# Performance work log

Measured on AMD Instinct MI355X. Metric: run time of the kernel, lower is better.

The kernel has to match this reference:

```python
import jax, jax.numpy as jnp
import numpy as np

N, E, IN_C, HID_C, OUT_C = 50000, 800000, 64, 64, 8
NEG_SLOPE = 0.2


def setup_inputs() -> dict:
    key = jax.random.key(0)
    ks = jax.random.split(key, 12)
    return {
        "x": jax.random.normal(ks[0], (N, IN_C), dtype=jnp.float32),
        "edge_index": jax.random.randint(ks[1], (2, E), 0, N, dtype=jnp.int64),
        "edge_value": jax.random.uniform(ks[2], (E,), dtype=jnp.float32),
        "W1": jax.random.normal(ks[3], (IN_C, HID_C), dtype=jnp.float32) * 0.1,
        "a1_src": jax.random.normal(ks[4], (HID_C,), dtype=jnp.float32) * 0.1,
        "a1_dst": jax.random.normal(ks[5], (HID_C,), dtype=jnp.float32) * 0.1,
        "b1": jnp.zeros((HID_C,), dtype=jnp.float32),
        "W2": jax.random.normal(ks[6], (HID_C, OUT_C), dtype=jnp.float32) * 0.1,
        "a2_src": jax.random.normal(ks[7], (OUT_C,), dtype=jnp.float32) * 0.1,
        "a2_dst": jax.random.normal(ks[8], (OUT_C,), dtype=jnp.float32) * 0.1,
        "b2": jnp.zeros((OUT_C,), dtype=jnp.float32),
    }


def _rgat_conv(x, src, dst, edge_value, W, a_src, a_dst, b, n_nodes):
    # Linear transform: [N, out_c]
    h = x @ W
    # Per-node attention halves, gathered per edge -> per-edge logit
    e_src = h @ a_src  # [N]
    e_dst = h @ a_dst  # [N]
    logits = jax.nn.leaky_relu(e_src[src] + e_dst[dst], negative_slope=NEG_SLOPE)  # [E]
    # Segment softmax over destination neighborhoods (numerically stable)
    m = jax.ops.segment_max(logits, dst, num_segments=n_nodes)  # [N]
    ex = jnp.exp(logits - m[dst])
    denom = jax.ops.segment_sum(ex, dst, num_segments=n_nodes)  # [N]
    alpha = ex / (denom[dst] + 1e-16)  # [E]
    # Edge-weighted messages, scatter-aggregate to destinations
    msg = (alpha * edge_value)[:, None] * h[src]  # [E, out_c]
    out = jax.ops.segment_sum(msg, dst, num_segments=n_nodes)  # [N, out_c]
    return out + b


def reference(x, edge_index, edge_value, W1, a1_src, a1_dst, b1, W2, a2_src, a2_dst, b2):
    src, dst = edge_index[0], edge_index[1]
    n = x.shape[0]
    hid = _rgat_conv(x, src, dst, edge_value, W1, a1_src, a1_dst, b1, n)
    hid = jax.nn.relu(hid)
    out = _rgat_conv(hid, src, dst, edge_value, W2, a2_src, a2_dst, b2, n)
    return jax.nn.log_softmax(out, axis=1)
```

## Files before the change

### kernel.cpp

```cpp
#include <hip/hip_runtime.h>
#include <hip/hip_fp16.h>
#include <math.h>


#define CHUNK 4096
#define NBKT  256
#define CAP   6144

typedef unsigned long long ull;
typedef float v2f __attribute__((ext_vector_type(2)));

struct PartSmem {
    int lhist[NBKT], lbase[NBKT], lcur[NBKT], gbase[NBKT];
    ull buf[CHUNK];
};
struct GemmSmem {
    float4 Wl[64 * 16];
    float  Xt[64 * 64];
};
union FusedSmem { PartSmem p; GemmSmem g; };


__global__ void __launch_bounds__(256) part_gemm_kernel(
    const int* __restrict__ src, const int* __restrict__ dst,
    const float* __restrict__ ev, int* __restrict__ bcnt,
    ull* __restrict__ ped, int E, int nchunks,
    const float* __restrict__ x, const float* __restrict__ W,
    const float* __restrict__ a_src, const float* __restrict__ a_dst,
    unsigned* __restrict__ h, float* __restrict__ es, float* __restrict__ ed,
    int N)
{
    __shared__ FusedSmem sm;
    const int t = threadIdx.x;

    if (blockIdx.x < nchunks) {
        int e0 = blockIdx.x * CHUNK;
        int cnt = min(CHUNK, E - e0);
        sm.p.lhist[t] = 0;
        __syncthreads();
        for (int i = t; i < cnt; i += 256)
            atomicAdd(&sm.p.lhist[dst[e0 + i] >> 8], 1);
        __syncthreads();
        int myc = sm.p.lhist[t];
        sm.p.lbase[t] = myc;
        __syncthreads();
        for (int o = 1; o < 256; o <<= 1) {
            int add = (t >= o) ? sm.p.lbase[t - o] : 0;
            __syncthreads();
            sm.p.lbase[t] += add;
            __syncthreads();
        }
        int excl = sm.p.lbase[t] - myc;
        sm.p.gbase[t] = myc ? atomicAdd(&bcnt[t], myc) : 0;
        __syncthreads();
        sm.p.lbase[t] = excl;
        sm.p.lcur[t] = excl;
        __syncthreads();
        for (int i = t; i < cnt; i += 256) {
            int e = e0 + i;
            int d = dst[e];
            int b = d >> 8;
            unsigned p = (unsigned)src[e] | ((unsigned)(d & 255) << 16)
                       | ((unsigned)b << 24);
            ull q = (ull)p | ((ull)__float_as_uint(ev[e]) << 32);
            int r = atomicAdd(&sm.p.lcur[b], 1);
            sm.p.buf[r] = q;
        }
        __syncthreads();
        for (int i = t; i < cnt; i += 256) {
            ull q = sm.p.buf[i];
            int b = (int)((q >> 24) & 255);
            ped[(size_t)b * CAP + sm.p.gbase[b] + i - sm.p.lbase[b]] = q;
        }
        return;
    }

    const int n0 = (blockIdx.x - nchunks) * 64;

    #pragma unroll
    for (int i = 0; i < 4; ++i)
        sm.g.Wl[t + i * 256] = ((const float4*)W)[t + i * 256];

    #pragma unroll
    for (int i = 0; i < 4; ++i) {
        int f   = t + i * 256;
        int row = f >> 4, kq = f & 15;
        int grow = n0 + row;
        float4 v = make_float4(0.f, 0.f, 0.f, 0.f);
        if (grow < N) v = ((const float4*)x)[(size_t)grow * 16 + kq];
        int rs = row ^ ((kq & 3) << 2);
        sm.g.Xt[(kq * 4 + 0) * 64 + rs] = v.x;
        sm.g.Xt[(kq * 4 + 1) * 64 + rs] = v.y;
        sm.g.Xt[(kq * 4 + 2) * 64 + rs] = v.z;
        sm.g.Xt[(kq * 4 + 3) * 64 + rs] = v.w;
    }

    const int tx = t & 15;
    const int ty = t >> 4;
    const float4 asv = ((const float4*)a_src)[tx];
    const float4 adv = ((const float4*)a_dst)[tx];
    __syncthreads();

    float4 acc0 = make_float4(0.f,0.f,0.f,0.f);
    float4 acc1 = make_float4(0.f,0.f,0.f,0.f);
    float4 acc2 = make_float4(0.f,0.f,0.f,0.f);
    float4 acc3 = make_float4(0.f,0.f,0.f,0.f);

    #pragma unroll 8
    for (int k = 0; k < 64; ++k) {
        int swz = (k >> 2) & 3;
        const float4 xr = *(const float4*)&sm.g.Xt[k * 64 + ((ty ^ swz) << 2)];
        const float4 wv = sm.g.Wl[k * 16 + tx];
        acc0.x += xr.x * wv.x; acc0.y += xr.x * wv.y;
        acc0.z += xr.x * wv.z; acc0.w += xr.x * wv.w;
        acc1.x += xr.y * wv.x; acc1.y += xr.y * wv.y;
        acc1.z += xr.y * wv.z; acc1.w += xr.y * wv.w;
        acc2.x += xr.z * wv.x; acc2.y += xr.z * wv.y;
        acc2.z += xr.z * wv.z; acc2.w += xr.z * wv.w;
        acc3.x += xr.w * wv.x; acc3.y += xr.w * wv.y;
        acc3.z += xr.w * wv.z; acc3.w += xr.w * wv.w;
    }

    float4 accs[4] = {acc0, acc1, acc2, acc3};
    #pragma unroll
    for (int r = 0; r < 4; ++r) {
        int grow = n0 + ty * 4 + r;
        float4 a = accs[r];
        if (grow < N) {
            int lo = __builtin_amdgcn_cvt_pk_fp8_f32(a.x, a.y, 0, false);
            int pk = __builtin_amdgcn_cvt_pk_fp8_f32(a.z, a.w, lo, true);
            h[(size_t)grow * 16 + tx] = (unsigned)pk;
        }
        float ps = a.x * asv.x + a.y * asv.y + a.z * asv.z + a.w * asv.w;
        float pd = a.x * adv.x + a.y * adv.y + a.z * adv.z + a.w * adv.w;
        #pragma unroll
        for (int o = 8; o > 0; o >>= 1) {
            ps += __shfl_xor(ps, o);
            pd += __shfl_xor(pd, o);
        }
        if (tx == 0 && grow < N) { es[grow] = ps; ed[grow] = pd; }
    }
}


__global__ void __launch_bounds__(1024) csr2_kernel(
    const ull* __restrict__ ped, const int* __restrict__ bcnt,
    int* __restrict__ off, int* __restrict__ deg,
    ull* __restrict__ csre, int N)
{
    __shared__ int cl[256], sc[256], cur[256];
    int b = blockIdx.x, t = threadIdx.x;
    const int cnt = min(bcnt[b], CAP);
    const size_t base = (size_t)b * CAP;
    if (t < 256) cl[t] = 0;
    __syncthreads();
    for (int i = t; i < cnt; i += 1024)
        atomicAdd(&cl[(int)((ped[base + i] >> 16) & 255)], 1);
    __syncthreads();
    int myc = (t < 256) ? cl[t] : 0;
    if (t < 256) sc[t] = myc;
    __syncthreads();
    for (int o = 1; o < 256; o <<= 1) {
        int add = (t >= o && t < 256) ? sc[t - o] : 0;
        __syncthreads();
        if (t < 256) sc[t] += add;
        __syncthreads();
    }
    if (t < 256) {
        int excl = sc[t] - myc;
        int node = b * 256 + t;
        if (node < N) { off[node] = (int)base + excl; deg[node] = myc; }
        cur[t] = excl;
    }
    __syncthreads();
    for (int i = t; i < cnt; i += 1024) {
        ull q = ped[base + i];
        int dloc = (int)((q >> 16) & 255);
        int pos = (int)base + atomicAdd(&cur[dloc], 1);
        csre[pos] = (q & 0xFFFFFFFF00000000ull) | (q & 0xFFFFull);
    }
}


__global__ void __launch_bounds__(256) agg64_fused_kernel(
    const int* __restrict__ off, const int* __restrict__ deg,
    const ull* __restrict__ csre,
    const float* __restrict__ es, const float* __restrict__ ed,
    const unsigned* __restrict__ h, const float* __restrict__ b1,
    const float* __restrict__ W2, const float* __restrict__ a2s,
    const float* __restrict__ a2d, float* __restrict__ h2,
    float* __restrict__ es2, float* __restrict__ ed2, int N)
{
    __shared__ float W2s[64 * 8];
    const int t = threadIdx.x;
    if (t < 128) ((float4*)W2s)[t] = ((const float4*)W2)[t];

    const int wid = t >> 6, lane = t & 63;
    const int grp = lane >> 2;
    const int sl  = lane & 3;
    const int gbase = grp << 2;
    const int n = (blockIdx.x * 4 + wid) * 16 + grp;
    __syncthreads();
    if (n >= N) return;

    const int   beg = off[n];
    const int   dg  = deg[n];
    const float edn = ed[n];

    const float4 b1v0 = *(const float4*)&b1[sl * 16];
    const float4 b1v1 = *(const float4*)&b1[sl * 16 + 4];
    const float4 b1v2 = *(const float4*)&b1[sl * 16 + 8];
    const float4 b1v3 = *(const float4*)&b1[sl * 16 + 12];

    float acc[16];
    #pragma unroll
    for (int k = 0; k < 16; ++k) acc[k] = 0.f;
    float den = 0.f;

    for (int j0 = 0; j0 < dg; j0 += 4) {
        const int jj  = j0 + sl;
        const ull rec = csre[beg + min(jj, dg - 1)];
        const int sv  = (int)(rec & 0xFFFFull);
        const float evv = __uint_as_float((unsigned)(rec >> 32));
        float z = es[sv] + edn;
        float l = z > 0.f ? z : 0.2f * z;
        float q = (jj < dg) ? __expf(l) : 0.f;
        den += q;
        const float w = q * evv;
        #pragma unroll
        for (int ts = 0; ts < 4; ++ts) {
            const int   svt = __shfl(sv, gbase + ts);
            const float wt  = __shfl(w,  gbase + ts);
            const uint4 u = *(const uint4*)&h[(size_t)svt * 16 + sl * 4];
            v2f fa = __builtin_amdgcn_cvt_pk_f32_fp8((int)u.x, false);
            v2f fb = __builtin_amdgcn_cvt_pk_f32_fp8((int)u.x, true);
            v2f fc = __builtin_amdgcn_cvt_pk_f32_fp8((int)u.y, false);
            v2f fd = __builtin_amdgcn_cvt_pk_f32_fp8((int)u.y, true);
            v2f fe = __builtin_amdgcn_cvt_pk_f32_fp8((int)u.z, false);
            v2f ff = __builtin_amdgcn_cvt_pk_f32_fp8((int)u.z, true);
            v2f fg = __builtin_amdgcn_cvt_pk_f32_fp8((int)u.w, false);
            v2f fh = __builtin_amdgcn_cvt_pk_f32_fp8((int)u.w, true);
            acc[0]  += wt * fa.x; acc[1]  += wt * fa.y;
            acc[2]  += wt * fb.x; acc[3]  += wt * fb.y;
            acc[4]  += wt * fc.x; acc[5]  += wt * fc.y;
            acc[6]  += wt * fd.x; acc[7]  += wt * fd.y;
            acc[8]  += wt * fe.x; acc[9]  += wt * fe.y;
            acc[10] += wt * ff.x; acc[11] += wt * ff.y;
            acc[12] += wt * fg.x; acc[13] += wt * fg.y;
            acc[14] += wt * fh.x; acc[15] += wt * fh.y;
        }
    }

    den += __shfl_xor(den, 1);
    den += __shfl_xor(den, 2);
    const float inv = 1.f / (den + 1e-16f);

    float hid[16];
    hid[0]  = fmaxf(acc[0]  * inv + b1v0.x, 0.f);
    hid[1]  = fmaxf(acc[1]  * inv + b1v0.y, 0.f);
    hid[2]  = fmaxf(acc[2]  * inv + b1v0.z, 0.f);
    hid[3]  = fmaxf(acc[3]  * inv + b1v0.w, 0.f);
    hid[4]  = fmaxf(acc[4]  * inv + b1v1.x, 0.f);
    hid[5]  = fmaxf(acc[5]  * inv + b1v1.y, 0.f);
    hid[6]  = fmaxf(acc[6]  * inv + b1v1.z, 0.f);
    hid[7]  = fmaxf(acc[7]  * inv + b1v1.w, 0.f);
    hid[8]  = fmaxf(acc[8]  * inv + b1v2.x, 0.f);
    hid[9]  = fmaxf(acc[9]  * inv + b1v2.y, 0.f);
    hid[10] = fmaxf(acc[10] * inv + b1v2.z, 0.f);
    hid[11] = fmaxf(acc[11] * inv + b1v2.w, 0.f);
    hid[12] = fmaxf(acc[12] * inv + b1v3.x, 0.f);
    hid[13] = fmaxf(acc[13] * inv + b1v3.y, 0.f);
    hid[14] = fmaxf(acc[14] * inv + b1v3.z, 0.f);
    hid[15] = fmaxf(acc[15] * inv + b1v3.w, 0.f);

    float p[8];
    #pragma unroll
    for (int o = 0; o < 8; ++o) p[o] = 0.f;
    #pragma unroll
    for (int k = 0; k < 16; ++k) {
        const float4 wA = *(const float4*)&W2s[(sl * 16 + k) * 8];
        const float4 wB = *(const float4*)&W2s[(sl * 16 + k) * 8 + 4];
        p[0] += hid[k] * wA.x; p[1] += hid[k] * wA.y;
        p[2] += hid[k] * wA.z; p[3] += hid[k] * wA.w;
        p[4] += hid[k] * wB.x; p[5] += hid[k] * wB.y;
        p[6] += hid[k] * wB.z; p[7] += hid[k] * wB.w;
    }
    float s4[4];
    {
        const bool hi = (sl & 1);
        #pragma unroll
        for (int k = 0; k < 4; ++k) {
            float keep = hi ? p[k + 4] : p[k];
            float send = hi ? p[k]     : p[k + 4];
            s4[k] = keep + __shfl_xor(send, 1);
        }
    }
    float s2[2];
    {
        const bool hi = (sl & 2);
        #pragma unroll
        for (int k = 0; k < 2; ++k) {
            float keep = hi ? s4[k + 2] : s4[k];
            float send = hi ? s4[k]     : s4[k + 2];
            s2[k] = keep + __shfl_xor(send, 2);
        }
    }
    const int oo = 4 * (sl & 1) + 2 * ((sl >> 1) & 1);

    float tsv = s2[0] * a2s[oo] + s2[1] * a2s[oo + 1];
    float tdv = s2[0] * a2d[oo] + s2[1] * a2d[oo + 1];
    tsv += __shfl_xor(tsv, 1); tdv += __shfl_xor(tdv, 1);
    tsv += __shfl_xor(tsv, 2); tdv += __shfl_xor(tdv, 2);

    *(float2*)&h2[(size_t)n * 8 + oo] = make_float2(s2[0], s2[1]);
    if (sl == 0) { es2[n] = tsv; ed2[n] = tdv; }
}


__global__ void __launch_bounds__(256) agg8_lsm_kernel(
    const int* __restrict__ off, const int* __restrict__ deg,
    const ull* __restrict__ csre,
    const float* __restrict__ es, const float* __restrict__ ed,
    const float* __restrict__ h2, const float* __restrict__ b,
    float* __restrict__ out, int N)
{
    const int t = threadIdx.x;
    const int wid = t >> 6, lane = t & 63;
    const int grp = lane >> 2;
    const int sl  = lane & 3;
    const int gbase = grp << 2;
    const int n = (blockIdx.x * 4 + wid) * 16 + grp;
    if (n >= N) return;

    const int   beg = off[n];
    const int   dg  = deg[n];
    const float edn = ed[n];
    const float bc0 = b[2 * sl], bc1 = b[2 * sl + 1];

    float a0 = 0.f, a1 = 0.f, den = 0.f;

    for (int j0 = 0; j0 < dg; j0 += 4) {
        const int jj  = j0 + sl;
        const ull rec = csre[beg + min(jj, dg - 1)];
        const int sv  = (int)(rec & 0xFFFFull);
        const float evv = __uint_as_float((unsigned)(rec >> 32));
        float z = es[sv] + edn;
        float l = z > 0.f ? z : 0.2f * z;
        float q = (jj < dg) ? __expf(l) : 0.f;
        den += q;
        const float w = q * evv;
        #pragma unroll
        for (int ts = 0; ts < 4; ++ts) {
            const int   svt = __shfl(sv, gbase + ts);
            const float wt  = __shfl(w,  gbase + ts);
            const float2 f = *(const float2*)&h2[(size_t)svt * 8 + 2 * sl];
            a0 += wt * f.x;
            a1 += wt * f.y;
        }
    }

    den += __shfl_xor(den, 1);
    den += __shfl_xor(den, 2);
    const float inv = 1.f / (den + 1e-16f);
    float v0 = a0 * inv + bc0;
    float v1 = a1 * inv + bc1;

    float vm = fmaxf(v0, v1);
    vm = fmaxf(vm, __shfl_xor(vm, 1));
    vm = fmaxf(vm, __shfl_xor(vm, 2));
    float s = __expf(v0 - vm) + __expf(v1 - vm);
    s += __shfl_xor(s, 1);
    s += __shfl_xor(s, 2);
    float lse = vm + logf(s);
    *(float2*)&out[(size_t)n * 8 + 2 * sl] = make_float2(v0 - lse, v1 - lse);
}


extern "C" void kernel_launch(void* const* d_in, const int* in_sizes, int n_in,
                              void* d_out, int out_size, void* d_ws, size_t ws_size,
                              hipStream_t stream)
{
    const float* x   = (const float*)d_in[0];
    const int*   ei  = (const int*)d_in[1];
    const float* ev  = (const float*)d_in[2];
    const float* W1  = (const float*)d_in[3];
    const float* a1s = (const float*)d_in[4];
    const float* a1d = (const float*)d_in[5];
    const float* b1  = (const float*)d_in[6];
    const float* W2  = (const float*)d_in[7];
    const float* a2s = (const float*)d_in[8];
    const float* a2d = (const float*)d_in[9];
    const float* b2  = (const float*)d_in[10];
    float* out = (float*)d_out;

    const int N = in_sizes[0] / 64;
    const int E = in_sizes[2];
    const int* srcp = ei;
    const int* dstp = ei + E;
    const int nchunks = (E + CHUNK - 1) / CHUNK;
    const int ngemm   = (N + 63) / 64;
    const int nbuck = (N + 255) / 256;

    ull*   ped  = (ull*)d_ws;
    ull*   csre = ped + (size_t)NBKT * CAP;
    int*   bcnt = (int*)(csre + (size_t)NBKT * CAP);
    int*   off  = bcnt + NBKT;
    int*   deg  = off + N;
    float* es1  = (float*)(deg + N);
    float* ed1  = es1 + N;
    float* es2  = ed1 + N;
    float* ed2  = es2 + N;
    unsigned* h1 = (unsigned*)(ed2 + N);
    float* h2   = (float*)(h1 + (size_t)N * 16);

    hipMemsetAsync(bcnt, 0, NBKT * sizeof(int), stream);

    part_gemm_kernel<<<nchunks + ngemm, 256, 0, stream>>>(
        srcp, dstp, ev, bcnt, ped, E, nchunks,
        x, W1, a1s, a1d, h1, es1, ed1, N);

    csr2_kernel<<<nbuck, 1024, 0, stream>>>(ped, bcnt, off, deg, csre, N);

    agg64_fused_kernel<<<(N + 63) / 64, 256, 0, stream>>>(
        off, deg, csre, es1, ed1, h1, b1, W2, a2s, a2d, h2, es2, ed2, N);

    agg8_lsm_kernel<<<(N + 63) / 64, 256, 0, stream>>>(
        off, deg, csre, es2, ed2, h2, b2, out, N);
}
```

Baseline: 140.4 us.

## Fuse CSR build with layer-1 aggregation and precompute edge weights per bucket

Merges the CSR-building kernel into the layer-1 aggregation kernel so that each 256-node bucket block builds its CSR slice, computes the attention exponentials and softmax denominators per edge with shared-memory atomics, and writes a packed (src, weight) array that the aggregation loop then reads. The layer-2 kernel is likewise reorganised per bucket: it computes edge weights and denominators into shared memory before aggregating. This drops one launch and removes the per-node redundant exp/es gather from the inner loops. In exchange the grid shrinks to about 196 blocks of 256 threads, which cuts parallelism and occupancy on a large GPU. The change also adds shared-memory float atomics and a 24KB shared buffer in the layer-2 kernel.

```diff
diff --git a/kernel.cpp b/kernel.cpp
--- a/kernel.cpp
+++ b/kernel.cpp
@@ -143,236 +143,261 @@
 }
 
 
-__global__ void __launch_bounds__(1024) csr2_kernel(
+__global__ void __launch_bounds__(256) csrw_agg64_kernel(
     const ull* __restrict__ ped, const int* __restrict__ bcnt,
+    const float* __restrict__ es1, const float* __restrict__ ed1,
     int* __restrict__ off, int* __restrict__ deg,
-    ull* __restrict__ csre, int N)
-{
-    __shared__ int cl[256], sc[256], cur[256];
-    int b = blockIdx.x, t = threadIdx.x;
-    const int cnt = min(bcnt[b], CAP);
-    const size_t base = (size_t)b * CAP;
-    if (t < 256) cl[t] = 0;
-    __syncthreads();
-    for (int i = t; i < cnt; i += 1024)
-        atomicAdd(&cl[(int)((ped[base + i] >> 16) & 255)], 1);
-    __syncthreads();
-    int myc = (t < 256) ? cl[t] : 0;
-    if (t < 256) sc[t] = myc;
-    __syncthreads();
-    for (int o = 1; o < 256; o <<= 1) {
-        int add = (t >= o && t < 256) ? sc[t - o] : 0;
-        __syncthreads();
-        if (t < 256) sc[t] += add;
-        __syncthreads();
-    }
-    if (t < 256) {
-        int excl = sc[t] - myc;
-        int node = b * 256 + t;
-        if (node < N) { off[node] = (int)base + excl; deg[node] = myc; }
-        cur[t] = excl;
-    }
-    __syncthreads();
-    for (int i = t; i < cnt; i += 1024) {
-        ull q = ped[base + i];
-        int dloc = (int)((q >> 16) & 255);
-        int pos = (int)base + atomicAdd(&cur[dloc], 1);
-        csre[pos] = (q & 0xFFFFFFFF00000000ull) | (q & 0xFFFFull);
-    }
-}
-
-
-__global__ void __launch_bounds__(256) agg64_fused_kernel(
-    const int* __restrict__ off, const int* __restrict__ deg,
-    const ull* __restrict__ csre,
-    const float* __restrict__ es, const float* __restrict__ ed,
-    const unsigned* __restrict__ h, const float* __restrict__ b1,
+    ull* __restrict__ csre, ull* __restrict__ csrw,
+    const unsigned* __restrict__ h1, const float* __restrict__ b1,
     const float* __restrict__ W2, const float* __restrict__ a2s,
     const float* __restrict__ a2d, float* __restrict__ h2,
     float* __restrict__ es2, float* __restrict__ ed2, int N)
 {
+    __shared__ int   lhist[256], lbase[256], lcur[256], degl[256];
+    __shared__ float den1[256], eds[256];
     __shared__ float W2s[64 * 8];
-    const int t = threadIdx.x;
+
+    const int b = blockIdx.x, t = threadIdx.x;
+    const int cnt = min(bcnt[b], CAP);
+    const size_t base = (size_t)b * CAP;
+    const int nodeT = b * 256 + t;
+
+    lhist[t] = 0;
+    den1[t] = 0.f;
+    eds[t] = (nodeT < N) ? ed1[nodeT] : 0.f;
     if (t < 128) ((float4*)W2s)[t] = ((const float4*)W2)[t];
+    __syncthreads();
+
+    for (int i = t; i < cnt; i += 256)
+        atomicAdd(&lhist[(int)((ped[base + i] >> 16) & 255)], 1);
+    __syncthreads();
+    int myc = lhist[t];
+    lbase[t] = myc;
+    __syncthreads();
+    for (int o = 1; o < 256; o <<= 1) {
+        int add = (t >= o) ? lbase[t - o] : 0;
+        __syncthreads();
+        lbase[t] += add;
+        __syncthreads();
+    }
+    const int excl = lbase[t] - myc;
+    lcur[t] = excl;
+    degl[t] = myc;
+    __syncthreads();
+    lbase[t] = excl;
+    if (nodeT < N) { off[nodeT] = (int)base + excl; deg[nodeT] = myc; }
+    __syncthreads();
+
+    for (int i = t; i < cnt; i += 256) {
+        const ull q = ped[base + i];
+        const int sv   = (int)(q & 0xFFFFull);
+        const int dloc = (int)((q >> 16) & 255);
+        const float evv = __uint_as_float((unsigned)(q >> 32));
+        float z = es1[sv] + eds[dloc];
+        float l = z > 0.f ? z : 0.2f * z;
+        float e = __expf(l);
+        atomicAdd(&den1[dloc], e);
+        const float w1 = e * evv;
+        const int pos = (int)base + atomicAdd(&lcur[dloc], 1);
+        csre[pos] = (q & 0xFFFFFFFF00000000ull) | ((ull)(unsigned)(dloc << 16))
+                  | (ull)(unsigned)sv;
+        csrw[pos] = ((ull)__float_as_uint(w1) << 32) | (ull)(unsigned)sv;
+    }
+    __syncthreads();
 
     const int wid = t >> 6, lane = t & 63;
-    const int grp = lane >> 2;
-    const int sl  = lane & 3;
-    const int gbase = grp << 2;
-    const int n = (blockIdx.x * 4 + wid) * 16 + grp;
-    __syncthreads();
-    if (n >= N) return;
-
-    const int   beg = off[n];
-    const int   dg  = deg[n];
-    const float edn = ed[n];
-
-    const float4 b1v0 = *(const float4*)&b1[sl * 16];
-    const float4 b1v1 = *(const float4*)&b1[sl * 16 + 4];
-    const float4 b1v2 = *(const float4*)&b1[sl * 16 + 8];
-    const float4 b1v3 = *(const float4*)&b1[sl * 16 + 12];
-
-    float acc[16];
+    const int grp = lane >> 2, sl = lane & 3, gbase = grp << 2;
+
     #pragma unroll
-    for (int k = 0; k < 16; ++k) acc[k] = 0.f;
-    float den = 0.f;
-
-    for (int j0 = 0; j0 < dg; j0 += 4) {
-        const int jj  = j0 + sl;
-        const ull rec = csre[beg + min(jj, dg - 1)];
-        const int sv  = (int)(rec & 0xFFFFull);
-        const float evv = __uint_as_float((unsigned)(rec >> 32));
-        float z = es[sv] + edn;
-        float l = z > 0.f ? z : 0.2f * z;
-        float q = (jj < dg) ? __expf(l) : 0.f;
-        den += q;
-        const float w = q * evv;
+    for (int pass = 0; pass < 4; ++pass) {
+        const int nloc = pass * 64 + wid * 16 + grp;
+        const int n = b * 256 + nloc;
+        if (n >= N) continue;
+
+        const int dg  = degl[nloc];
+        const int beg = (int)base + lbase[nloc];
+
+        float acc[16];
         #pragma unroll
-        for (int ts = 0; ts < 4; ++ts) {
-            const int   svt = __shfl(sv, gbase + ts);
-            const float wt  = __shfl(w,  gbase + ts);
-            const uint4 u = *(const uint4*)&h[(size_t)svt * 16 + sl * 4];
-            v2f fa = __builtin_amdgcn_cvt_pk_f32_fp8((int)u.x, false);
-            v2f fb = __builtin_amdgcn_cvt_pk_f32_fp8((int)u.x, true);
-            v2f fc = __builtin_amdgcn_cvt_pk_f32_fp8((int)u.y, false);
-            v2f fd = __builtin_amdgcn_cvt_pk_f32_fp8((int)u.y, true);
-            v2f fe = __builtin_amdgcn_cvt_pk_f32_fp8((int)u.z, false);
-            v2f ff = __builtin_amdgcn_cvt_pk_f32_fp8((int)u.z, true);
-            v2f fg = __builtin_amdgcn_cvt_pk_f32_fp8((int)u.w, false);
-            v2f fh = __builtin_amdgcn_cvt_pk_f32_fp8((int)u.w, true);
-            acc[0]  += wt * fa.x; acc[1]  += wt * fa.y;
-            acc[2]  += wt * fb.x; acc[3]  += wt * fb.y;
-            acc[4]  += wt * fc.x; acc[5]  += wt * fc.y;
-            acc[6]  += wt * fd.x; acc[7]  += wt * fd.y;
-            acc[8]  += wt * fe.x; acc[9]  += wt * fe.y;
-            acc[10] += wt * ff.x; acc[11] += wt * ff.y;
-            acc[12] += wt * fg.x; acc[13] += wt * fg.y;
-            acc[14] += wt * fh.x; acc[15] += wt * fh.y;
-        }
-    }
-
-    den += __shfl_xor(den, 1);
-    den += __shfl_xor(den, 2);
-    const float inv = 1.f / (den + 1e-16f);
-
-    float hid[16];
-    hid[0]  = fmaxf(acc[0]  * inv + b1v0.x, 0.f);
-    hid[1]  = fmaxf(acc[1]  * inv + b1v0.y, 0.f);
-    hid[2]  = fmaxf(acc[2]  * inv + b1v0.z, 0.f);
-    hid[3]  = fmaxf(acc[3]  * inv + b1v0.w, 0.f);
-    hid[4]  = fmaxf(acc[4]  * inv + b1v1.x, 0.f);
-    hid[5]  = fmaxf(acc[5]  * inv + b1v1.y, 0.f);
-    hid[6]  = fmaxf(acc[6]  * inv + b1v1.z, 0.f);
-    hid[7]  = fmaxf(acc[7]  * inv + b1v1.w, 0.f);
-    hid[8]  = fmaxf(acc[8]  * inv + b1v2.x, 0.f);
-    hid[9]  = fmaxf(acc[9]  * inv + b1v2.y, 0.f);
-    hid[10] = fmaxf(acc[10] * inv + b1v2.z, 0.f);
-    hid[11] = fmaxf(acc[11] * inv + b1v2.w, 0.f);
-    hid[12] = fmaxf(acc[12] * inv + b1v3.x, 0.f);
-    hid[13] = fmaxf(acc[13] * inv + b1v3.y, 0.f);
-    hid[14] = fmaxf(acc[14] * inv + b1v3.z, 0.f);
-    hid[15] = fmaxf(acc[15] * inv + b1v3.w, 0.f);
-
-    float p[8];
-    #pragma unroll
-    for (int o = 0; o < 8; ++o) p[o] = 0.f;
-    #pragma unroll
-    for (int k = 0; k < 16; ++k) {
-        const float4 wA = *(const float4*)&W2s[(sl * 16 + k) * 8];
-        const float4 wB = *(const float4*)&W2s[(sl * 16 + k) * 8 + 4];
-        p[0] += hid[k] * wA.x; p[1] += hid[k] * wA.y;
-        p[2] += hid[k] * wA.z; p[3] += hid[k] * wA.w;
-        p[4] += hid[k] * wB.x; p[5] += hid[k] * wB.y;
-        p[6] += hid[k] * wB.z; p[7] += hid[k] * wB.w;
-    }
-    float s4[4];
-    {
-        const bool hi = (sl & 1);
+        for (int k = 0; k < 16; ++k) acc[k] = 0.f;
+
+        for (int j0 = 0; j0 < dg; j0 += 4) {
+            const int jj  = j0 + sl;
+            const ull rec = csrw[beg + min(jj, dg - 1)];
+            const int sv  = (int)(rec & 0xFFFFull);
+            float w = __uint_as_float((unsigned)(rec >> 32));
+            w = (jj < dg) ? w : 0.f;
+            #pragma unroll
+            for (int ts = 0; ts < 4; ++ts) {
+                const int   svt = __shfl(sv, gbase + ts);
+                const float wt  = __shfl(w,  gbase + ts);
+                const uint4 u = *(const uint4*)&h1[(size_t)svt * 16 + sl * 4];
+                v2f fa = __builtin_amdgcn_cvt_pk_f32_fp8((int)u.x, false);
+                v2f fb = __builtin_amdgcn_cvt_pk_f32_fp8((int)u.x, true);
+                v2f fc = __builtin_amdgcn_cvt_pk_f32_fp8((int)u.y, false);
+                v2f fd = __builtin_amdgcn_cvt_pk_f32_fp8((int)u.y, true);
+                v2f fe = __builtin_amdgcn_cvt_pk_f32_fp8((int)u.z, false);
+                v2f ff = __builtin_amdgcn_cvt_pk_f32_fp8((int)u.z, true);
+                v2f fg = __builtin_amdgcn_cvt_pk_f32_fp8((int)u.w, false);
+                v2f fh = __builtin_amdgcn_cvt_pk_f32_fp8((int)u.w, true);
+                acc[0]  += wt * fa.x; acc[1]  += wt * fa.y;
+                acc[2]  += wt * fb.x; acc[3]  += wt * fb.y;
+                acc[4]  += wt * fc.x; acc[5]  += wt * fc.y;
+                acc[6]  += wt * fd.x; acc[7]  += wt * fd.y;
+                acc[8]  += wt * fe.x; acc[9]  += wt * fe.y;
+                acc[10] += wt * ff.x; acc[11] += wt * ff.y;
+                acc[12] += wt * fg.x; acc[13] += wt * fg.y;
+                acc[14] += wt * fh.x; acc[15] += wt * fh.y;
+            }
+        }
+
+        const float inv = 1.f / (den1[nloc] + 1e-16f);
+
+        const float4 b1v0 = *(const float4*)&b1[sl * 16];
+        const float4 b1v1 = *(const float4*)&b1[sl * 16 + 4];
+        const float4 b1v2 = *(const float4*)&b1[sl * 16 + 8];
+        const float4 b1v3 = *(const float4*)&b1[sl * 16 + 12];
+
+        float hid[16];
+        hid[0]  = fmaxf(acc[0]  * inv + b1v0.x, 0.f);
+        hid[1]  = fmaxf(acc[1]  * inv + b1v0.y, 0.f);
+        hid[2]  = fmaxf(acc[2]  * inv + b1v0.z, 0.f);
+        hid[3]  = fmaxf(acc[3]  * inv + b1v0.w, 0.f);
+        hid[4]  = fmaxf(acc[4]  * inv + b1v1.x, 0.f);
+        hid[5]  = fmaxf(acc[5]  * inv + b1v1.y, 0.f);
+        hid[6]  = fmaxf(acc[6]  * inv + b1v1.z, 0.f);
+        hid[7]  = fmaxf(acc[7]  * inv + b1v1.w, 0.f);
+        hid[8]  = fmaxf(acc[8]  * inv + b1v2.x, 0.f);
+        hid[9]  = fmaxf(acc[9]  * inv + b1v2.y, 0.f);
+        hid[10] = fmaxf(acc[10] * inv + b1v2.z, 0.f);
+        hid[11] = fmaxf(acc[11] * inv + b1v2.w, 0.f);
+        hid[12] = fmaxf(acc[12] * inv + b1v3.x, 0.f);
+        hid[13] = fmaxf(acc[13] * inv + b1v3.y, 0.f);
+        hid[14] = fmaxf(acc[14] * inv + b1v3.z, 0.f);
+        hid[15] = fmaxf(acc[15] * inv + b1v3.w, 0.f);
+
+        float p[8];
         #pragma unroll
-        for (int k = 0; k < 4; ++k) {
-            float keep = hi ? p[k + 4] : p[k];
-            float send = hi ? p[k]     : p[k + 4];
-            s4[k] = keep + __shfl_xor(send, 1);
-        }
-    }
-    float s2[2];
-    {
-        const bool hi = (sl & 2);
+        for (int o = 0; o < 8; ++o) p[o] = 0.f;
         #pragma unroll
-        for (int k = 0; k < 2; ++k) {
-            float keep = hi ? s4[k + 2] : s4[k];
-            float send = hi ? s4[k]     : s4[k + 2];
-            s2[k] = keep + __shfl_xor(send, 2);
-        }
-    }
-    const int oo = 4 * (sl & 1) + 2 * ((sl >> 1) & 1);
-
-    float tsv = s2[0] * a2s[oo] + s2[1] * a2s[oo + 1];
-    float tdv = s2[0] * a2d[oo] + s2[1] * a2d[oo + 1];
-    tsv += __shfl_xor(tsv, 1); tdv += __shfl_xor(tdv, 1);
-    tsv += __shfl_xor(tsv, 2); tdv += __shfl_xor(tdv, 2);
-
-    *(float2*)&h2[(size_t)n * 8 + oo] = make_float2(s2[0], s2[1]);
-    if (sl == 0) { es2[n] = tsv; ed2[n] = tdv; }
+        for (int k = 0; k < 16; ++k) {
+            const float4 wA = *(const float4*)&W2s[(sl * 16 + k) * 8];
+            const float4 wB = *(const float4*)&W2s[(sl * 16 + k) * 8 + 4];
+            p[0] += hid[k] * wA.x; p[1] += hid[k] * wA.y;
+            p[2] += hid[k] * wA.z; p[3] += hid[k] * wA.w;
+            p[4] += hid[k] * wB.x; p[5] += hid[k] * wB.y;
+            p[6] += hid[k] * wB.z; p[7] += hid[k] * wB.w;
+        }
+        float s4[4];
+        {
+            const bool hi = (sl & 1);
+            #pragma unroll
+            for (int k = 0; k < 4; ++k) {
+                float keep = hi ? p[k + 4] : p[k];
+                float send = hi ? p[k]     : p[k + 4];
+                s4[k] = keep + __shfl_xor(send, 1);
+            }
+        }
+        float s2[2];
+        {
+            const bool hi = (sl & 2);
+            #pragma unroll
+            for (int k = 0; k < 2; ++k) {
+                float keep = hi ? s4[k + 2] : s4[k];
+                float send = hi ? s4[k]     : s4[k + 2];
+                s2[k] = keep + __shfl_xor(send, 2);
+            }
+        }
+        const int oo = 4 * (sl & 1) + 2 * ((sl >> 1) & 1);
+
+        float tsv = s2[0] * a2s[oo] + s2[1] * a2s[oo + 1];
+        float tdv = s2[0] * a2d[oo] + s2[1] * a2d[oo + 1];
+        tsv += __shfl_xor(tsv, 1); tdv += __shfl_xor(tdv, 1);
+        tsv += __shfl_xor(tsv, 2); tdv += __shfl_xor(tdv, 2);
+
+        *(float2*)&h2[(size_t)n * 8 + oo] = make_float2(s2[0], s2[1]);
+        if (sl == 0) { es2[n] = tsv; ed2[n] = tdv; }
+    }
 }
 
 
 __global__ void __launch_bounds__(256) agg8_lsm_kernel(
-    const int* __restrict__ off, const int* __restrict__ deg,
-    const ull* __restrict__ csre,
-    const float* __restrict__ es, const float* __restrict__ ed,
-    const float* __restrict__ h2, const float* __restrict__ b,
+    const int* __restrict__ bcnt, const int* __restrict__ off,
+    const int* __restrict__ deg, const ull* __restrict__ csre,
+    const float* __restrict__ es2, const float* __restrict__ ed2,
+    const float* __restrict__ h2, const float* __restrict__ b2,
     float* __restrict__ out, int N)
 {
-    const int t = threadIdx.x;
+    __shared__ float w2v[CAP];
+    __shared__ float den2[256], ed2s[256];
+
+    const int b = blockIdx.x, t = threadIdx.x;
+    const int cnt = min(bcnt[b], CAP);
+    const size_t base = (size_t)b * CAP;
+    const int nodeT = b * 256 + t;
+
+    den2[t] = 0.f;
+    ed2s[t] = (nodeT < N) ? ed2[nodeT] : 0.f;
+    __syncthreads();
+
+    for (int i = t; i < cnt; i += 256) {
+        const ull r = csre[base + i];
+        const int sv   = (int)(r & 0xFFFFull);
+        const int dloc = (int)((r >> 16) & 255);
+        const float evv = __uint_as_float((unsigned)(r >> 32));
+        float z = es2[sv] + ed2s[dloc];
+        float l = z > 0.f ? z : 0.2f * z;
+        float q = __expf(l);
+        atomicAdd(&den2[dloc], q);
+        w2v[i] = q * evv;
+    }
+    __syncthreads();
+
     const int wid = t >> 6, lane = t & 63;
-    const int grp = lane >> 2;
-    const int sl  = lane & 3;
-    const int gbase = grp << 2;
-    const int n = (blockIdx.x * 4 + wid) * 16 + grp;
-    if (n >= N) return;
-
-    const int   beg = off[n];
-    const int   dg  = deg[n];
-    const float edn = ed[n];
-    const float bc0 = b[2 * sl], bc1 = b[2 * sl + 1];
-
-    float a0 = 0.f, a1 = 0.f, den = 0.f;
-
-    for (int j0 = 0; j0 < dg; j0 += 4) {
-        const int jj  = j0 + sl;
-        const ull rec = csre[beg + min(jj, dg - 1)];
-        const int sv  = (int)(rec & 0xFFFFull);
-        const float evv = __uint_as_float((unsigned)(rec >> 32));
-        float z = es[sv] + edn;
-        float l = z > 0.f ? z : 0.2f * z;
-        float q = (jj < dg) ? __expf(l) : 0.f;
-        den += q;
-        const float w = q * evv;
-        #pragma unroll
-        for (int ts = 0; ts < 4; ++ts) {
-            const int   svt = __shfl(sv, gbase + ts);
-            const float wt  = __shfl(w,  gbase + ts);
-            const float2 f = *(const float2*)&h2[(size_t)svt * 8 + 2 * sl];
-            a0 += wt * f.x;
-            a1 += wt * f.y;
-        }
-    }
-
-    den += __shfl_xor(den, 1);
-    den += __shfl_xor(den, 2);
-    const float inv = 1.f / (den + 1e-16f);
-    float v0 = a0 * inv + bc0;
-    float v1 = a1 * inv + bc1;
-
-    float vm = fmaxf(v0, v1);
-    vm = fmaxf(vm, __shfl_xor(vm, 1));
-    vm = fmaxf(vm, __shfl_xor(vm, 2));
-    float s = __expf(v0 - vm) + __expf(v1 - vm);
-    s += __shfl_xor(s, 1);
-    s += __shfl_xor(s, 2);
-    float lse = vm + logf(s);
-    *(float2*)&out[(size_t)n * 8 + 2 * sl] = make_float2(v0 - lse, v1 - lse);
+    const int grp = lane >> 2, sl = lane & 3, gbase = grp << 2;
+
+    #pragma unroll
+    for (int pass = 0; pass < 4; ++pass) {
+        const int nloc = pass * 64 + wid * 16 + grp;
+        const int n = b * 256 + nloc;
+        if (n >= N) continue;
+
+        const int beg = off[n];
+        const int dg  = deg[n];
+        const int lofs = beg - (int)base;
+
+        float a0 = 0.f, a1 = 0.f;
+
+        for (int j0 = 0; j0 < dg; j0 += 4) {
+            const int jj  = j0 + sl;
+            const int lidx = lofs + min(jj, dg - 1);
+            const ull r = csre[base + lidx];
+            const int sv = (int)(r & 0xFFFFull);
+            float w = w2v[lidx];
+            w = (jj < dg) ? w : 0.f;
+            #pragma unroll
+            for (int ts = 0; ts < 4; ++ts) {
+                const int   svt = __shfl(sv, gbase + ts);
+                const float wt  = __shfl(w,  gbase + ts);
+                const float2 f = *(const float2*)&h2[(size_t)svt * 8 + 2 * sl];
+                a0 += wt * f.x;
+                a1 += wt * f.y;
+            }
+        }
+
+        const float inv = 1.f / (den2[nloc] + 1e-16f);
+        float v0 = a0 * inv + b2[2 * sl];
+        float v1 = a1 * inv + b2[2 * sl + 1];
+
+        float vm = fmaxf(v0, v1);
+        vm = fmaxf(vm, __shfl_xor(vm, 1));
+        vm = fmaxf(vm, __shfl_xor(vm, 2));
+        float s = __expf(v0 - vm) + __expf(v1 - vm);
+        s += __shfl_xor(s, 1);
+        s += __shfl_xor(s, 2);
+        float lse = vm + logf(s);
+        *(float2*)&out[(size_t)n * 8 + 2 * sl] = make_float2(v0 - lse, v1 - lse);
+    }
 }
 
 
@@ -399,11 +424,12 @@
     const int* dstp = ei + E;
     const int nchunks = (E + CHUNK - 1) / CHUNK;
     const int ngemm   = (N + 63) / 64;
-    const int nbuck = (N + 255) / 256;
+    const int nbuck   = (N + 255) / 256;
 
     ull*   ped  = (ull*)d_ws;
     ull*   csre = ped + (size_t)NBKT * CAP;
-    int*   bcnt = (int*)(csre + (size_t)NBKT * CAP);
+    ull*   csrw = csre + (size_t)NBKT * CAP;
+    int*   bcnt = (int*)(csrw + (size_t)NBKT * CAP);
     int*   off  = bcnt + NBKT;
     int*   deg  = off + N;
     float* es1  = (float*)(deg + N);
@@ -419,11 +445,10 @@
         srcp, dstp, ev, bcnt, ped, E, nchunks,
         x, W1, a1s, a1d, h1, es1, ed1, N);
 
-    csr2_kernel<<<nbuck, 1024, 0, stream>>>(ped, bcnt, off, deg, csre, N);
-
-    agg64_fused_kernel<<<(N + 63) / 64, 256, 0, stream>>>(
-        off, deg, csre, es1, ed1, h1, b1, W2, a2s, a2d, h2, es2, ed2, N);
-
-    agg8_lsm_kernel<<<(N + 63) / 64, 256, 0, stream>>>(
-        off, deg, csre, es2, ed2, h2, b2, out, N);
+    csrw_agg64_kernel<<<nbuck, 256, 0, stream>>>(
+        ped, bcnt, es1, ed1, off, deg, csre, csrw,
+        h1, b1, W2, a2s, a2d, h2, es2, ed2, N);
+
+    agg8_lsm_kernel<<<nbuck, 256, 0, stream>>>(
+        bcnt, off, deg, csre, es2, ed2, h2, b2, out, N);
 }
```

Result: slower. 166.4 us (+18.5%).
